# Optimization experiments

Measured on AMD Instinct MI355X. Metric: run time of the kernel, lower is better.

Reference implementation:

```python
import jax, jax.numpy as jnp
import numpy as np

N = 262144          # total points
C = 16              # classes
AVG_DEG = 16
E = N * AVG_DEG     # edges
LAMBDA1 = 0.7
LAMBDA2 = 0.5
LAMBDA_S = 0.2
LOSS_WEIGHT = 1.0
IGNORE_INDEX = -1
EPS = 1e-8


def setup_inputs() -> dict:
    key = jax.random.key(0)
    k1, k2, k3, k4 = jax.random.split(key, 4)
    pred = jax.random.normal(k1, (N, C), dtype=jnp.float32)
    target = jax.random.randint(k2, (N,), 0, C, dtype=jnp.int64)
    # precomputed radius-graph edge list (row = destination, col = source)
    row = jax.random.randint(k3, (E,), 0, N, dtype=jnp.int64)
    col = jax.random.randint(k4, (E,), 0, N, dtype=jnp.int64)
    return {"pred": pred, "target": target, "row": row, "col": col}


def _masked_mean(x, mask):
    cnt = jnp.sum(mask.astype(x.dtype))
    s = jnp.sum(jnp.where(mask, x, jnp.zeros_like(x)))
    return jnp.where(cnt > 0, s / jnp.maximum(cnt, 1.0), s)


def reference(pred, target, row, col):
    # per-point CE (reduction='none'); ignored points contribute 0
    log_probs = jax.nn.log_softmax(pred, axis=1)          # [N, C]
    probs = jnp.exp(log_probs)                            # [N, C]
    valid_mask = target != IGNORE_INDEX
    tgt = jnp.where(valid_mask, target, 0)
    ce_per_point = -jnp.take_along_axis(log_probs, tgt[:, None], axis=1)[:, 0]
    ce_per_point = jnp.where(valid_mask, ce_per_point, 0.0)

    conf = jnp.max(probs, axis=1)                         # [N]
    pred_label = jnp.argmax(probs, axis=1)                # [N]

    # degree per destination node
    deg = jax.ops.segment_sum(jnp.ones((E,), dtype=probs.dtype), row, num_segments=N)

    # neighborhood agreement u_i = mean_{j in N(i)} [pred_j == pred_i]
    agree_edge = (pred_label[col] == pred_label[row]).astype(probs.dtype)
    sum_agree = jax.ops.segment_sum(agree_edge, row, num_segments=N)
    u = jnp.where(deg > 0, sum_agree / jnp.maximum(deg, 1.0), jnp.ones_like(sum_agree))

    w = 1.0 + LAMBDA1 * (1.0 - u) + LAMBDA2 * (1.0 - conf)
    loss_ce = _masked_mean(w * ce_per_point, valid_mask)

    # per-edge KL(p_i || p_j) with clamp at 1e-8, scatter-mean over neighbors
    pi = probs[row]                                       # [E, C]
    pj = probs[col]                                       # [E, C]
    kl_edge = jnp.sum(
        pi * (jnp.log(jnp.maximum(pi, EPS)) - jnp.log(jnp.maximum(pj, EPS))), axis=1
    )                                                     # [E]
    sum_kl = jax.ops.segment_sum(kl_edge, row, num_segments=N)
    mean_kl = jnp.where(deg > 0, sum_kl / jnp.maximum(deg, 1.0), jnp.zeros_like(sum_kl))
    loss_smooth = _masked_mean(mean_kl, valid_mask)

    return (loss_ce + LAMBDA_S * loss_smooth) * LOSS_WEIGHT
```

## Files before the change

### kernel.cpp

```cpp
#include <hip/hip_runtime.h>

constexpr float LAMBDA1  = 0.7f;
constexpr float LAMBDA2  = 0.5f;
constexpr float LAMBDA_S = 0.2f;
constexpr float LOG_EPS  = -18.420680743952367f;
constexpr float PQ_SCALE  = 15.0f;
constexpr float LQ_SCALE4 = 15.0f / 18.420680743952367f;
constexpr float DOT_SCALE4 = 18.420680743952367f / (15.0f * 15.0f);

constexpr int      BUCK_SHIFT = 10;
constexpr unsigned BUCK_CAP   = 20480u;
constexpr int      CHUNK      = 8192;
constexpr int      FT         = 1024;
constexpr int      CUR_PAD    = 16;
constexpr int      NB_NODE    = 256;

#if defined(__has_builtin)
#if __has_builtin(__builtin_amdgcn_udot8)
#define HAS_UDOT8 1
#endif
#endif

__global__ void __launch_bounds__(FT, 8)
k_fused(const float* __restrict__ pred,
        const int*   __restrict__ target,
        unsigned long long* __restrict__ probsQ4,
        unsigned long long* __restrict__ logpQ4,
        float* __restrict__ Hn,
        float* __restrict__ confn,
        float* __restrict__ cen,
        const int* __restrict__ row,
        const int* __restrict__ col,
        unsigned* __restrict__ bucketed,
        unsigned* __restrict__ gcursor,
        int n, int e, int bucketBlocks) {
    int t = threadIdx.x;

    if ((int)blockIdx.x < bucketBlocks) {
        __shared__ unsigned stage[CHUNK];
        __shared__ unsigned char bid[CHUNK];
        __shared__ unsigned hist[256];
        __shared__ unsigned cnt[256];
        __shared__ unsigned lofs[256];
        __shared__ unsigned baseArr[256];

        if (t < 256) { hist[t] = 0; cnt[t] = 0; }
        __syncthreads();

        long i0 = (long)blockIdx.x * CHUNK;
        int chunkN = (int)(((long)e - i0) < CHUNK ? ((long)e - i0) : CHUNK);
        if (chunkN < 0) chunkN = 0;

        for (int k = t; k < chunkN; k += FT) {
            int r = __builtin_nontemporal_load(row + i0 + k);
            atomicAdd(&hist[r >> BUCK_SHIFT], 1u);
        }
        __syncthreads();

        if (t < 64) {
            unsigned h0 = hist[4 * t], h1 = hist[4 * t + 1],
                     h2 = hist[4 * t + 2], h3 = hist[4 * t + 3];
            unsigned s = h0 + h1 + h2 + h3;
            unsigned inc = s;
#pragma unroll
            for (int off = 1; off < 64; off <<= 1) {
                unsigned v = __shfl_up(inc, off, 64);
                if (t >= off) inc += v;
            }
            unsigned run = inc - s;
            lofs[4 * t]     = run;
            lofs[4 * t + 1] = run + h0;
            lofs[4 * t + 2] = run + h0 + h1;
            lofs[4 * t + 3] = run + h0 + h1 + h2;
#pragma unroll
            for (int j = 0; j < 4; ++j) {
                int b = 4 * t + j;
                unsigned h = hist[b];
                baseArr[b] = (unsigned)b * BUCK_CAP
                           + atomicAdd(&gcursor[b * CUR_PAD], h);
            }
        }
        __syncthreads();

        for (int k = t; k < chunkN; k += FT) {
            int r = row[i0 + k];
            int c = __builtin_nontemporal_load(col + i0 + k);
            int b = r >> BUCK_SHIFT;
            unsigned s = lofs[b] + atomicAdd(&cnt[b], 1u);
            stage[s] = ((unsigned)(r & 1023) << 18) | (unsigned)c;
            bid[s]   = (unsigned char)b;
        }
        __syncthreads();

        for (int k = t; k < chunkN; k += FT) {
            unsigned b   = bid[k];
            unsigned dst = baseArr[b] + ((unsigned)k - lofs[b]);
            if (dst < (b + 1) * BUCK_CAP)
                bucketed[dst] = stage[k];
        }
    } else {
        int i = (blockIdx.x - bucketBlocks) * FT + t;
        if (i >= n) return;

        const float4* p4 = reinterpret_cast<const float4*>(pred + (size_t)i * 16);
        float4 v0 = p4[0], v1 = p4[1], v2 = p4[2], v3 = p4[3];
        float x[16] = {v0.x, v0.y, v0.z, v0.w,
                       v1.x, v1.y, v1.z, v1.w,
                       v2.x, v2.y, v2.z, v2.w,
                       v3.x, v3.y, v3.z, v3.w};

        float m = x[0];
#pragma unroll
        for (int c = 1; c < 16; ++c) m = fmaxf(m, x[c]);

        float s = 0.f;
#pragma unroll
        for (int c = 0; c < 16; ++c) s += __expf(x[c] - m);
        float logZ = m + __logf(s);

        unsigned long long pq64 = 0ull, lq64 = 0ull;
        float Hacc = 0.f;
#pragma unroll
        for (int c = 0; c < 16; ++c) {
            float lp  = x[c] - logZ;
            float p   = __expf(lp);
            float lpc = fmaxf(lp, LOG_EPS);
            Hacc += p * lpc;

            unsigned pq = (unsigned)(int)rintf(p * PQ_SCALE);
            unsigned lq = (unsigned)(int)rintf(-lpc * LQ_SCALE4);
            pq64 |= (unsigned long long)pq << (4 * c);
            lq64 |= (unsigned long long)lq << (4 * c);
        }

        probsQ4[i] = pq64;
        logpQ4[i]  = lq64;

        Hn[i]    = Hacc;
        confn[i] = __expf(m - logZ);

        int tt0 = target[i];
        bool valid = (tt0 != -1);
        int tt = valid ? tt0 : 0;
        float xt = x[0];
#pragma unroll
        for (int c = 1; c < 16; ++c) xt = (c == tt) ? x[c] : xt;
        cen[i] = valid ? -(xt - logZ) : 0.f;
    }
}

__global__ void k_reduce(const unsigned* __restrict__ bucketed,
                         const unsigned* __restrict__ gcursor,
                         const unsigned long long* __restrict__ probsQ4,
                         const unsigned long long* __restrict__ logpQ4,
                         unsigned long long* __restrict__ accPart,
                         int n) {
    __shared__ unsigned long long acc[1024];
    __shared__ unsigned long long Ptab[1024];
    __shared__ unsigned char labr[1024];
    int t = threadIdx.x;
    int b = blockIdx.x >> 2;
    int q = blockIdx.x & 3;

    for (int i = t; i < 1024; i += 256) {
        acc[i] = 0ull;
        int node = (b << BUCK_SHIFT) + i;
        unsigned long long P = (node < n) ? probsQ4[node] : 0ull;
        Ptab[i] = P;
        unsigned plo = (unsigned)P, phi = (unsigned)(P >> 32);
        int lr = 0, mr = -1;
#pragma unroll
        for (int k2 = 0; k2 < 8; ++k2) {
            int pv = (int)((plo >> (4 * k2)) & 15u);
            if (pv > mr) { mr = pv; lr = k2; }
        }
#pragma unroll
        for (int k2 = 0; k2 < 8; ++k2) {
            int pv = (int)((phi >> (4 * k2)) & 15u);
            if (pv > mr) { mr = pv; lr = 8 + k2; }
        }
        labr[i] = (unsigned char)lr;
    }
    __syncthreads();

    unsigned nb = gcursor[b * CUR_PAD];
    if (nb > BUCK_CAP) nb = BUCK_CAP;
    unsigned s0 = (nb * (unsigned)q) >> 2;
    unsigned s1 = (nb * (unsigned)(q + 1)) >> 2;
    unsigned base = (unsigned)b * BUCK_CAP;

    for (unsigned k = s0 + (unsigned)t; k < s1; k += 256) {
        unsigned pl = bucketed[base + k];
        unsigned c  = pl & 0x3FFFFu;
        unsigned lr = pl >> 18;
        unsigned long long P = Ptab[lr];
        unsigned long long L = logpQ4[c];
        unsigned plo = (unsigned)P, phi = (unsigned)(P >> 32);
        unsigned llo = (unsigned)L, lhi = (unsigned)(L >> 32);

        unsigned dot;
#ifdef HAS_UDOT8
        dot = __builtin_amdgcn_udot8(plo, llo, 0u, false);
        dot = __builtin_amdgcn_udot8(phi, lhi, dot, false);
#else
        dot = 0;
#pragma unroll
        for (int k2 = 0; k2 < 8; ++k2) {
            dot += ((plo >> (4 * k2)) & 15u) * ((llo >> (4 * k2)) & 15u);
            dot += ((phi >> (4 * k2)) & 15u) * ((lhi >> (4 * k2)) & 15u);
        }
#endif
        int lab_c = 0, mc = 1000;
#pragma unroll
        for (int k2 = 0; k2 < 8; ++k2) {
            int lv = (int)((llo >> (4 * k2)) & 15u);
            if (lv < mc) { mc = lv; lab_c = k2; }
        }
#pragma unroll
        for (int k2 = 0; k2 < 8; ++k2) {
            int lv = (int)((lhi >> (4 * k2)) & 15u);
            if (lv < mc) { mc = lv; lab_c = 8 + k2; }
        }

        unsigned agree = ((int)labr[lr] == lab_c) ? 1u : 0u;
        unsigned long long add =
            ((unsigned long long)(0x10000u | agree) << 32)
            | (unsigned long long)dot;
        atomicAdd(&acc[lr], add);
    }
    __syncthreads();

    for (int i = t; i < 1024; i += 256) {
        int node = (b << BUCK_SHIFT) + i;
        if (node < n) accPart[(size_t)q * n + node] = acc[i];
    }
}

__global__ void k_node(const int* __restrict__ target,
                       const float* __restrict__ confn,
                       const float* __restrict__ cen,
                       const float* __restrict__ Hn,
                       const unsigned long long* __restrict__ accPart,
                       float* __restrict__ partial,
                       int n) {
    float wce = 0.f, mkl = 0.f, v = 0.f;
    for (int i = blockIdx.x * blockDim.x + threadIdx.x; i < n;
         i += gridDim.x * blockDim.x) {
        unsigned long long pk = 0ull;
#pragma unroll
        for (int qx = 0; qx < 4; ++qx)
            pk += accPart[(size_t)qx * n + i];
        float deg  = (float)(unsigned)(pk >> 48);
        float sag  = (float)(unsigned)((pk >> 32) & 0xFFFFu);
        float sdot = (float)(unsigned)(pk & 0xFFFFFFFFull);
        float u  = (deg > 0.f) ? sag / deg : 1.f;
        float mk = (deg > 0.f) ? (Hn[i] + sdot * DOT_SCALE4 / deg) : 0.f;
        float w  = 1.f + LAMBDA1 * (1.f - u) + LAMBDA2 * (1.f - confn[i]);
        int t = target[i];
        if (t != -1) {
            wce += w * cen[i];
            mkl += mk;
            v   += 1.f;
        }
    }
#pragma unroll
    for (int off = 32; off > 0; off >>= 1) {
        wce += __shfl_down(wce, off, 64);
        mkl += __shfl_down(mkl, off, 64);
        v   += __shfl_down(v,   off, 64);
    }
    __shared__ float s[3][4];
    int wave = threadIdx.x >> 6, lane = threadIdx.x & 63;
    if (lane == 0) { s[0][wave] = wce; s[1][wave] = mkl; s[2][wave] = v; }
    __syncthreads();
    if (threadIdx.x == 0) {
        float a = 0.f, bb = 0.f, c = 0.f;
#pragma unroll
        for (int w = 0; w < 4; ++w) { a += s[0][w]; bb += s[1][w]; c += s[2][w]; }
        float4* p4 = reinterpret_cast<float4*>(partial);
        p4[blockIdx.x] = make_float4(a, bb, c, 0.f);
    }
}

__global__ void k_final(const float* __restrict__ partial, float* __restrict__ out) {
    int t = threadIdx.x;
    const float4* p4 = reinterpret_cast<const float4*>(partial);
    float4 pv = p4[t];
    float wce = pv.x, mkl = pv.y, v = pv.z;
#pragma unroll
    for (int off = 32; off > 0; off >>= 1) {
        wce += __shfl_down(wce, off, 64);
        mkl += __shfl_down(mkl, off, 64);
        v   += __shfl_down(v,   off, 64);
    }
    __shared__ float s[3][4];
    int wave = t >> 6, lane = t & 63;
    if (lane == 0) { s[0][wave] = wce; s[1][wave] = mkl; s[2][wave] = v; }
    __syncthreads();
    if (t == 0) {
        float a = 0.f, b = 0.f, c = 0.f;
#pragma unroll
        for (int w = 0; w < 4; ++w) { a += s[0][w]; b += s[1][w]; c += s[2][w]; }
        float lce = (c > 0.f) ? a / fmaxf(c, 1.f) : a;
        float ls  = (c > 0.f) ? b / fmaxf(c, 1.f) : b;
        out[0] = lce + LAMBDA_S * ls;
    }
}

extern "C" void kernel_launch(void* const* d_in, const int* in_sizes, int n_in,
                              void* d_out, int out_size, void* d_ws, size_t ws_size,
                              hipStream_t stream) {
    const float* pred   = (const float*)d_in[0];
    const int*   target = (const int*)d_in[1];
    const int*   row    = (const int*)d_in[2];
    const int*   col    = (const int*)d_in[3];
    float* out = (float*)d_out;

    const int n = in_sizes[1];
    const int e = in_sizes[2];

    const int nbuck = (n + 1023) >> BUCK_SHIFT;
    const int bucketBlocks = (e + CHUNK - 1) / CHUNK;
    const int pointBlocks  = (n + FT - 1) / FT;

    char* base = (char*)d_ws;
    size_t off = 0;
    unsigned long long* probsQ4 = (unsigned long long*)(base + off); off += (size_t)n * 8;
    unsigned long long* logpQ4  = (unsigned long long*)(base + off); off += (size_t)n * 8;
    float* Hn     = (float*)(base + off); off += (size_t)n * sizeof(float);
    float* confn  = (float*)(base + off); off += (size_t)n * sizeof(float);
    float* cen    = (float*)(base + off); off += (size_t)n * sizeof(float);
    unsigned* bucketed = (unsigned*)(base + off); off += (size_t)nbuck * BUCK_CAP * 4;
    unsigned* gcursor  = (unsigned*)(base + off); off += (size_t)nbuck * CUR_PAD * 4;
    unsigned long long* accPart = (unsigned long long*)(base + off); off += (size_t)4 * n * 8;
    float* partial = (float*)(base + off); off += (size_t)NB_NODE * 4 * sizeof(float);

    hipMemsetAsync(gcursor, 0, (size_t)nbuck * CUR_PAD * 4, stream);

    const int B = 256;
    k_fused<<<bucketBlocks + pointBlocks, FT, 0, stream>>>(
        pred, target, probsQ4, logpQ4, Hn, confn, cen,
        row, col, bucketed, gcursor, n, e, bucketBlocks);
    k_reduce<<<nbuck * 4, B, 0, stream>>>(bucketed, gcursor, probsQ4, logpQ4,
                                          accPart, n);
    k_node<<<NB_NODE, B, 0, stream>>>(target, confn, cen, Hn,
                                      accPart, partial, n);
    k_final<<<1, B, 0, stream>>>(partial, out);
}
```

Measured before the change: 150.4 us.

## Fuse per-node loss reduction into bucket reduce kernel with one block per bucket

Each bucket is now handled by a single 1024-thread block instead of four 256-thread blocks, so per-node accumulators stay complete in shared memory. The per-node weight/KL computation and block partial sum are done in the same kernel, removing the accPart global buffer and the k_node launch. This cuts one kernel launch and a round trip of 4*n 64-bit partials through memory. In exchange there are fewer blocks (nbuck=256) and longer edge loops per block, which may reduce parallelism and latency hiding.

```diff
diff --git a/kernel.cpp b/kernel.cpp
--- a/kernel.cpp
+++ b/kernel.cpp
@@ -12,8 +12,8 @@
 constexpr unsigned BUCK_CAP   = 20480u;
 constexpr int      CHUNK      = 8192;
 constexpr int      FT         = 1024;
+constexpr int      RT         = 1024;
 constexpr int      CUR_PAD    = 16;
-constexpr int      NB_NODE    = 256;
 
 #if defined(__has_builtin)
 #if __has_builtin(__builtin_amdgcn_udot8)
@@ -149,24 +149,29 @@
     }
 }
 
-__global__ void k_reduce(const unsigned* __restrict__ bucketed,
-                         const unsigned* __restrict__ gcursor,
-                         const unsigned long long* __restrict__ probsQ4,
-                         const unsigned long long* __restrict__ logpQ4,
-                         unsigned long long* __restrict__ accPart,
-                         int n) {
+__global__ void __launch_bounds__(RT)
+k_reduce(const unsigned* __restrict__ bucketed,
+         const unsigned* __restrict__ gcursor,
+         const unsigned long long* __restrict__ probsQ4,
+         const unsigned long long* __restrict__ logpQ4,
+         const int*   __restrict__ target,
+         const float* __restrict__ confn,
+         const float* __restrict__ cen,
+         const float* __restrict__ Hn,
+         float* __restrict__ partial,
+         int n) {
     __shared__ unsigned long long acc[1024];
     __shared__ unsigned long long Ptab[1024];
     __shared__ unsigned char labr[1024];
+    __shared__ float sred[3][16];
     int t = threadIdx.x;
-    int b = blockIdx.x >> 2;
-    int q = blockIdx.x & 3;
-
-    for (int i = t; i < 1024; i += 256) {
-        acc[i] = 0ull;
-        int node = (b << BUCK_SHIFT) + i;
+    int b = blockIdx.x;
+
+    {
+        acc[t] = 0ull;
+        int node = (b << BUCK_SHIFT) + t;
         unsigned long long P = (node < n) ? probsQ4[node] : 0ull;
-        Ptab[i] = P;
+        Ptab[t] = P;
         unsigned plo = (unsigned)P, phi = (unsigned)(P >> 32);
         int lr = 0, mr = -1;
 #pragma unroll
@@ -179,17 +184,15 @@
             int pv = (int)((phi >> (4 * k2)) & 15u);
             if (pv > mr) { mr = pv; lr = 8 + k2; }
         }
-        labr[i] = (unsigned char)lr;
+        labr[t] = (unsigned char)lr;
     }
     __syncthreads();
 
     unsigned nb = gcursor[b * CUR_PAD];
     if (nb > BUCK_CAP) nb = BUCK_CAP;
-    unsigned s0 = (nb * (unsigned)q) >> 2;
-    unsigned s1 = (nb * (unsigned)(q + 1)) >> 2;
     unsigned base = (unsigned)b * BUCK_CAP;
 
-    for (unsigned k = s0 + (unsigned)t; k < s1; k += 256) {
+    for (unsigned k = (unsigned)t; k < nb; k += RT) {
         unsigned pl = bucketed[base + k];
         unsigned c  = pl & 0x3FFFFu;
         unsigned lr = pl >> 18;
@@ -230,37 +233,23 @@
     }
     __syncthreads();
 
-    for (int i = t; i < 1024; i += 256) {
-        int node = (b << BUCK_SHIFT) + i;
-        if (node < n) accPart[(size_t)q * n + node] = acc[i];
-    }
-}
-
-__global__ void k_node(const int* __restrict__ target,
-                       const float* __restrict__ confn,
-                       const float* __restrict__ cen,
-                       const float* __restrict__ Hn,
-                       const unsigned long long* __restrict__ accPart,
-                       float* __restrict__ partial,
-                       int n) {
     float wce = 0.f, mkl = 0.f, v = 0.f;
-    for (int i = blockIdx.x * blockDim.x + threadIdx.x; i < n;
-         i += gridDim.x * blockDim.x) {
-        unsigned long long pk = 0ull;
-#pragma unroll
-        for (int qx = 0; qx < 4; ++qx)
-            pk += accPart[(size_t)qx * n + i];
-        float deg  = (float)(unsigned)(pk >> 48);
-        float sag  = (float)(unsigned)((pk >> 32) & 0xFFFFu);
-        float sdot = (float)(unsigned)(pk & 0xFFFFFFFFull);
-        float u  = (deg > 0.f) ? sag / deg : 1.f;
-        float mk = (deg > 0.f) ? (Hn[i] + sdot * DOT_SCALE4 / deg) : 0.f;
-        float w  = 1.f + LAMBDA1 * (1.f - u) + LAMBDA2 * (1.f - confn[i]);
-        int t = target[i];
-        if (t != -1) {
-            wce += w * cen[i];
-            mkl += mk;
-            v   += 1.f;
+    {
+        int node = (b << BUCK_SHIFT) + t;
+        if (node < n) {
+            unsigned long long pk = acc[t];
+            float deg  = (float)(unsigned)(pk >> 48);
+            float sag  = (float)(unsigned)((pk >> 32) & 0xFFFFu);
+            float sdot = (float)(unsigned)(pk & 0xFFFFFFFFull);
+            float u  = (deg > 0.f) ? sag / deg : 1.f;
+            float mk = (deg > 0.f) ? (Hn[node] + sdot * DOT_SCALE4 / deg) : 0.f;
+            float w  = 1.f + LAMBDA1 * (1.f - u) + LAMBDA2 * (1.f - confn[node]);
+            int tg = target[node];
+            if (tg != -1) {
+                wce = w * cen[node];
+                mkl = mk;
+                v   = 1.f;
+            }
         }
     }
 #pragma unroll
@@ -269,16 +258,21 @@
         mkl += __shfl_down(mkl, off, 64);
         v   += __shfl_down(v,   off, 64);
     }
-    __shared__ float s[3][4];
-    int wave = threadIdx.x >> 6, lane = threadIdx.x & 63;
-    if (lane == 0) { s[0][wave] = wce; s[1][wave] = mkl; s[2][wave] = v; }
+    int wave = t >> 6, lane = t & 63;
+    if (lane == 0) { sred[0][wave] = wce; sred[1][wave] = mkl; sred[2][wave] = v; }
     __syncthreads();
-    if (threadIdx.x == 0) {
-        float a = 0.f, bb = 0.f, c = 0.f;
-#pragma unroll
-        for (int w = 0; w < 4; ++w) { a += s[0][w]; bb += s[1][w]; c += s[2][w]; }
-        float4* p4 = reinterpret_cast<float4*>(partial);
-        p4[blockIdx.x] = make_float4(a, bb, c, 0.f);
+    if (t < 16) {
+        float a = sred[0][t], bb = sred[1][t], c = sred[2][t];
+#pragma unroll
+        for (int off = 8; off > 0; off >>= 1) {
+            a  += __shfl_down(a,  off, 64);
+            bb += __shfl_down(bb, off, 64);
+            c  += __shfl_down(c,  off, 64);
+        }
+        if (t == 0) {
+            float4* p4 = reinterpret_cast<float4*>(partial);
+            p4[b] = make_float4(a, bb, c, 0.f);
+        }
     }
 }
 
@@ -332,18 +326,14 @@
     float* cen    = (float*)(base + off); off += (size_t)n * sizeof(float);
     unsigned* bucketed = (unsigned*)(base + off); off += (size_t)nbuck * BUCK_CAP * 4;
     unsigned* gcursor  = (unsigned*)(base + off); off += (size_t)nbuck * CUR_PAD * 4;
-    unsigned long long* accPart = (unsigned long long*)(base + off); off += (size_t)4 * n * 8;
-    float* partial = (float*)(base + off); off += (size_t)NB_NODE * 4 * sizeof(float);
+    float* partial = (float*)(base + off); off += (size_t)nbuck * 4 * sizeof(float);
 
     hipMemsetAsync(gcursor, 0, (size_t)nbuck * CUR_PAD * 4, stream);
 
-    const int B = 256;
     k_fused<<<bucketBlocks + pointBlocks, FT, 0, stream>>>(
         pred, target, probsQ4, logpQ4, Hn, confn, cen,
         row, col, bucketed, gcursor, n, e, bucketBlocks);
-    k_reduce<<<nbuck * 4, B, 0, stream>>>(bucketed, gcursor, probsQ4, logpQ4,
-                                          accPart, n);
-    k_node<<<NB_NODE, B, 0, stream>>>(target, confn, cen, Hn,
-                                      accPart, partial, n);
-    k_final<<<1, B, 0, stream>>>(partial, out);
+    k_reduce<<<nbuck, RT, 0, stream>>>(bucketed, gcursor, probsQ4, logpQ4,
+                                       target, confn, cen, Hn, partial, n);
+    k_final<<<1, 256, 0, stream>>>(partial, out);
 }
```

New measurement: 142.2 us. 5.4% less time.
